# Optimization experiments

Hardware: AMD Instinct MI355X
Metric: run time of the kernel (lower is better)

Reference implementation:

```python
import jax, jax.numpy as jnp
import numpy as np

EMBED_DIM = 1024
NUM_HEADS = 16
HEAD_DIM = EMBED_DIM // NUM_HEADS
SCALE = HEAD_DIM ** -0.5
B, S = 2, 2048


def setup_inputs() -> dict:
    key = jax.random.key(0)
    ks = jax.random.split(key, 11)
    lim = 1.0 / np.sqrt(EMBED_DIM)
    def lin(kw, kb):
        W = jax.random.uniform(kw, (EMBED_DIM, EMBED_DIM), jnp.float32, -lim, lim)
        b = jax.random.uniform(kb, (EMBED_DIM,), jnp.float32, -lim, lim)
        return W, b
    Wq, bq = lin(ks[0], ks[1])
    Wk, bk = lin(ks[2], ks[3])
    Wv, bv = lin(ks[4], ks[5])
    Wo, bo = lin(ks[6], ks[7])
    query = jax.random.normal(ks[8], (B, S, EMBED_DIM), jnp.float32)
    key_t = jax.random.normal(ks[9], (B, S, EMBED_DIM), jnp.float32)
    value = jax.random.normal(ks[10], (B, S, EMBED_DIM), jnp.float32)
    return {"query": query, "key": key_t, "value": value,
            "Wq": Wq, "bq": bq, "Wk": Wk, "bk": bk,
            "Wv": Wv, "bv": bv, "Wo": Wo, "bo": bo}


def reference(query, key, value, Wq, bq, Wk, bk, Wv, bv, Wo, bo):
    # 'flash' path with attn_mask=None == full softmax attention (chunking is
    # only an execution schedule; per-chunk softmax is over the full key axis).
    b, s, _ = query.shape
    def heads(x, W, bias):
        y = x @ W.T + bias                      # [b, s, E]
        return y.reshape(b, s, NUM_HEADS, HEAD_DIM).transpose(0, 2, 1, 3)  # [b, h, s, d]
    q = heads(query, Wq, bq)
    k = heads(key, Wk, bk)
    v = heads(value, Wv, bv)
    scores = jnp.einsum('bhqd,bhkd->bhqk', q, k) * SCALE
    attn = jax.nn.softmax(scores, axis=-1)
    out = jnp.einsum('bhqk,bhkd->bhqd', attn, v)
    out = out.transpose(0, 2, 1, 3).reshape(b, s, EMBED_DIM)
    return out @ Wo.T + bo
```

## Files before the change

### kernel.cpp

```cpp
#include <hip/hip_runtime.h>

typedef unsigned short u16;
typedef unsigned int u32;
typedef __attribute__((ext_vector_type(8))) __bf16 bf16x8;
typedef __attribute__((ext_vector_type(4))) float f32x4;
typedef __attribute__((ext_vector_type(4))) unsigned short u16x4;
typedef __attribute__((ext_vector_type(8))) unsigned short u16x8;
typedef __attribute__((ext_vector_type(4))) unsigned int u32x4;

#define DEV static __device__ __forceinline__

DEV void async_copy16(const void* g, void* l) {
  __builtin_amdgcn_global_load_lds((const __attribute__((address_space(1))) void*)g,
                                   (__attribute__((address_space(3))) void*)l, 16, 0, 0);
}
DEV float b2f(u16 s) { union { unsigned u; float f; } v; v.u = ((unsigned)s) << 16; return v.f; }
DEV u16 f2b(float f) {
  union { float f; unsigned u; } v; v.f = f;
  unsigned r = v.u + 0x7FFFu + ((v.u >> 16) & 1u);
  return (u16)(r >> 16);
}
DEV u32 pack2bf(float a, float b) {
  u32 ua = __float_as_uint(a) + 0x8000u;
  u32 ub = __float_as_uint(b) + 0x8000u;
  return __builtin_amdgcn_perm(ub, ua, 0x07060302u);
}

#define MFMA(a, b, c) __builtin_amdgcn_mfma_f32_16x16x32_bf16((a), (b), (c), 0, 0, 0)

__global__ void detect_dtype(const unsigned* __restrict__ q, int* __restrict__ flag) {
  const int lane = threadIdx.x;
  const unsigned w = q[lane];
  const unsigned e = (w >> 7) & 0xFFu;
  const bool inr = (e >= 100u && e <= 132u);
  const unsigned long long m = __ballot(inr);
  if (lane == 0) flag[0] = (__popcll(m) >= 48) ? 1 : 0;
}

__global__ void convert_inputs(
    const void* s0, const void* s1, const void* s2,
    const void* s3, const void* s4, const void* s5, const void* s6,
    const void* s7, const void* s8, const void* s9, const void* s10,
    u16* __restrict__ d0, u16* __restrict__ d1, u16* __restrict__ d2,
    u16* __restrict__ d3, u16* __restrict__ d4, u16* __restrict__ d5, u16* __restrict__ d6,
    float* __restrict__ e7, float* __restrict__ e8, float* __restrict__ e9, float* __restrict__ e10,
    const int* __restrict__ flag)
{
  const int bi = blockIdx.y;
  const void* src = nullptr; u16* db = nullptr; float* df = nullptr; int n = 0;
  switch (bi) {
    case 0:  src = s0;  db = d0; n = 4194304; break;
    case 1:  src = s1;  db = d1; n = 4194304; break;
    case 2:  src = s2;  db = d2; n = 4194304; break;
    case 3:  src = s3;  db = d3; n = 1048576; break;
    case 4:  src = s4;  db = d4; n = 1048576; break;
    case 5:  src = s5;  db = d5; n = 1048576; break;
    case 6:  src = s6;  db = d6; n = 1048576; break;
    case 7:  src = s7;  df = e7; n = 1024; break;
    case 8:  src = s8;  df = e8; n = 1024; break;
    case 9:  src = s9;  df = e9; n = 1024; break;
    default: src = s10; df = e10; n = 1024; break;
  }
  const int isbf = flag[0];
  const int stride = gridDim.x * 256 * 8;
  for (int i = (blockIdx.x * 256 + threadIdx.x) * 8; i < n; i += stride) {
    if (db) {
      u16x8 v;
      if (isbf) {
        v = *(const u16x8*)((const u16*)src + i);
      } else {
        const float* sf = (const float*)src;
#pragma unroll
        for (int j = 0; j < 8; ++j) v[j] = f2b(sf[i + j]);
      }
      *(u16x8*)(db + i) = v;
    } else {
#pragma unroll
      for (int j = 0; j < 8; ++j) {
        float x = isbf ? b2f(((const u16*)src)[i + j]) : ((const float*)src)[i + j];
        df[i + j] = x;
      }
    }
  }
}

__global__ void gemm_qkv(const u16* __restrict__ X0, const u16* __restrict__ X1, const u16* __restrict__ X2,
                         const u16* __restrict__ W0, const u16* __restrict__ W1, const u16* __restrict__ W2,
                         const float* __restrict__ B0, const float* __restrict__ B1, const float* __restrict__ B2,
                         u16* __restrict__ Y0, u16* __restrict__ Y1, u16* __restrict__ Y2,
                         float* __restrict__ Yf, const int* __restrict__ flag, int mode0)
{
  __shared__ __align__(16) u16 smem[17408];
  u16* As = smem;
  u16* Bs = smem + 4096;

  const int z = blockIdx.z;
  const u16* X  = (z == 0) ? X0 : ((z == 1) ? X1 : X2);
  const u16* W  = (z == 0) ? W0 : ((z == 1) ? W1 : W2);
  const float* Bi = (z == 0) ? B0 : ((z == 1) ? B1 : B2);
  u16* Y        = (z == 0) ? Y0 : ((z == 1) ? Y1 : Y2);
  const int mode = mode0 ? mode0 : z;
  const int outbf = flag[0];

  const int t = threadIdx.x, wave = t >> 6, lane = t & 63;
  const int lane15 = lane & 15, quad = lane >> 4;
  const int m0 = blockIdx.y * 128, n0 = blockIdx.x * 128;

  const u16* gA = X + (size_t)(m0 + wave * 16 + (lane >> 2)) * 1024 + (lane & 3) * 8;
  const u16* gB = W + (size_t)(n0 + wave * 16 + (lane >> 2)) * 1024 + (lane & 3) * 8;
  u16* lA = &As[wave * 16 * 32];
  u16* lB = &Bs[wave * 16 * 32];

  f32x4 acc[4][4];
#pragma unroll
  for (int i = 0; i < 4; ++i)
#pragma unroll
    for (int j = 0; j < 4; ++j) acc[i][j] = (f32x4){0.f, 0.f, 0.f, 0.f};

  const int wr = wave >> 1, wc = wave & 1;

  for (int k0 = 0; k0 < 1024; k0 += 32) {
    async_copy16(gA, lA);
    async_copy16(gA + 64 * 1024, lA + 64 * 32);
    async_copy16(gB, lB);
    async_copy16(gB + 64 * 1024, lB + 64 * 32);
    gA += 32; gB += 32;
    __syncthreads();

    bf16x8 af[4], bfv[4];
#pragma unroll
    for (int mt = 0; mt < 4; ++mt)
      af[mt] = *(const bf16x8*)&As[(wr * 64 + mt * 16 + lane15) * 32 + quad * 8];
#pragma unroll
    for (int nt = 0; nt < 4; ++nt)
      bfv[nt] = *(const bf16x8*)&Bs[(wc * 64 + nt * 16 + lane15) * 32 + quad * 8];
#pragma unroll
    for (int mt = 0; mt < 4; ++mt)
#pragma unroll
      for (int nt = 0; nt < 4; ++nt)
        acc[mt][nt] = MFMA(af[mt], bfv[nt], acc[mt][nt]);
    __syncthreads();
  }

  const float qscale = 0.125f * 1.44269504088896340736f;

  if (mode == 2) {
    u16* T2 = smem;
    __syncthreads();
#pragma unroll
    for (int mt = 0; mt < 4; ++mt) {
      const int sl_base = wr * 64 + mt * 16 + quad * 4;
#pragma unroll
      for (int nt = 0; nt < 4; ++nt) {
        const int nn = wc * 64 + nt * 16 + lane15;
        const float bias_v = Bi[n0 + nn];
#pragma unroll
        for (int r = 0; r < 4; ++r) {
          const int sl = sl_base + r;
          const int sp = ((sl & 15) << 3) | (sl >> 4);
          T2[nn * 136 + sp] = f2b(acc[mt][nt][r] + bias_v);
        }
      }
    }
    __syncthreads();
    const size_t grow0 = (size_t)(m0 >> 11) * 1024 + n0;
    const int col0 = m0 & 2047;
#pragma unroll
    for (int i = 0; i < 8; ++i) {
      const int id = i * 256 + t;
      const int row = id >> 4, ch = id & 15;
      *(u16x8*)&Y[(grow0 + row) * 2048 + col0 + ch * 8] = *(const u16x8*)&T2[row * 136 + ch * 8];
    }
    return;
  }

#pragma unroll
  for (int mt = 0; mt < 4; ++mt) {
    const int m_base = m0 + wr * 64 + mt * 16 + quad * 4;
#pragma unroll
    for (int nt = 0; nt < 4; ++nt) {
      const int n = n0 + wc * 64 + nt * 16 + lane15;
      const float bias_v = Bi[n];
#pragma unroll
      for (int r = 0; r < 4; ++r) {
        const int m = m_base + r;
        float v = acc[mt][nt][r] + bias_v;
        if (mode == 0) v *= qscale;
        if (mode == 3) {
          if (outbf) Y[(size_t)m * 1024 + n] = f2b(v);
          else       Yf[(size_t)m * 1024 + n] = v;
        } else {
          size_t addr = (((size_t)(m >> 11) * 16 + (n >> 6)) * 2048 + (size_t)(m & 2047)) * 64 + (n & 63);
          Y[addr] = f2b(v);
        }
      }
    }
  }
}

__global__ __launch_bounds__(256, 2) void flash_attn(const u16* __restrict__ Qs, const u16* __restrict__ Ks,
                                                     const u16* __restrict__ Vt, u16* __restrict__ AO)
{
  __shared__ __align__(16) u16 smem[32768];
  u16* Kt = smem;
  u16* Vs = smem + 8192;

  const int t = threadIdx.x, wave = t >> 6, lane = t & 63;
  const int lane15 = lane & 15, quad = lane >> 4;
  const int l7 = lane15 & 7;
  const int bh = blockIdx.y;
  const int q0 = blockIdx.x * 128;
  u16* Pw = smem + 16384 + wave * 4096;

  const u16* Qb = Qs + ((size_t)bh * 2048 + q0) * 64;
  const u16* Kb = Ks + (size_t)bh * 2048 * 64;
  const u16* Vb = Vt + (size_t)bh * 64 * 2048;

  const int krow = lane >> 3;
  const int kchunk = (lane & 7) ^ (krow & 7);
  const int vrow = lane >> 4;
  const int vchunk = (lane & 15) ^ (((wave & 1) << 2) + vrow);

#pragma unroll
  for (int r = 0; r < 4; ++r)
    async_copy16(Qb + (size_t)(r * 32 + wave * 8 + krow) * 64 + kchunk * 8,
                 &Kt[(r * 32 + wave * 8) * 64]);
  __syncthreads();
  bf16x8 aq[2][2];
#pragma unroll
  for (int mt = 0; mt < 2; ++mt)
#pragma unroll
    for (int ks = 0; ks < 2; ++ks)
      aq[mt][ks] = *(const bf16x8*)&Kt[(wave * 32 + mt * 16 + lane15) * 64 + ((ks * 4 + quad) ^ l7) * 8];
  __syncthreads();

  f32x4 acc_o[2][4], acc_l[2];
#pragma unroll
  for (int mt = 0; mt < 2; ++mt) {
    acc_l[mt] = (f32x4){0.f, 0.f, 0.f, 0.f};
#pragma unroll
    for (int i = 0; i < 4; ++i) acc_o[mt][i] = (f32x4){0.f, 0.f, 0.f, 0.f};
  }

  u16x8 ou;
#pragma unroll
  for (int j = 0; j < 8; ++j) ou[j] = 0x3F80;
  const bf16x8 ones = __builtin_bit_cast(bf16x8, ou);

  for (int kt = 0; kt < 16; ++kt) {
#pragma unroll
    for (int r = 0; r < 4; ++r)
      async_copy16(Kb + (size_t)(kt * 128 + r * 32 + wave * 8 + krow) * 64 + kchunk * 8,
                   &Kt[(r * 32 + wave * 8) * 64]);
#pragma unroll
    for (int r = 0; r < 4; ++r)
      async_copy16(Vb + (size_t)(r * 16 + wave * 4 + vrow) * 2048 + kt * 128 + vchunk * 8,
                   &Vs[(r * 16 + wave * 4) * 128]);
    __syncthreads();

    f32x4 s[2][8];
#pragma unroll
    for (int mt = 0; mt < 2; ++mt)
#pragma unroll
      for (int nt = 0; nt < 8; ++nt) s[mt][nt] = (f32x4){0.f, 0.f, 0.f, 0.f};
#pragma unroll
    for (int ks = 0; ks < 2; ++ks) {
      bf16x8 bk[8];
#pragma unroll
      for (int nt = 0; nt < 8; ++nt)
        bk[nt] = *(const bf16x8*)&Kt[(nt * 16 + lane15) * 64 + ((ks * 4 + quad) ^ l7) * 8];
#pragma unroll
      for (int mt = 0; mt < 2; ++mt)
#pragma unroll
        for (int nt = 0; nt < 8; ++nt)
          s[mt][nt] = MFMA(aq[mt][ks], bk[nt], s[mt][nt]);
    }

#pragma unroll
    for (int mt = 0; mt < 2; ++mt)
#pragma unroll
      for (int rg = 0; rg < 4; ++rg) {
        u32x4 w;
#pragma unroll
        for (int j = 0; j < 4; ++j)
          w[j] = pack2bf(__builtin_amdgcn_exp2f(s[mt][2 * j][rg]),
                         __builtin_amdgcn_exp2f(s[mt][2 * j + 1][rg]));
        const int r = mt * 16 + quad * 4 + rg;
        *(u32x4*)&Pw[r * 128 + (lane15 ^ (r & 7)) * 8] = w;
      }
    __threadfence_block();

#pragma unroll
    for (int ks2 = 0; ks2 < 4; ++ks2) {
      bf16x8 bv[4], ap[2];
#pragma unroll
      for (int dt = 0; dt < 4; ++dt)
        bv[dt] = *(const bf16x8*)&Vs[(dt * 16 + lane15) * 128 + ((ks2 * 4 + quad) ^ l7) * 8];
#pragma unroll
      for (int mt = 0; mt < 2; ++mt)
        ap[mt] = *(const bf16x8*)&Pw[(mt * 16 + lane15) * 128 + ((ks2 * 4 + quad) ^ l7) * 8];
#pragma unroll
      for (int mt = 0; mt < 2; ++mt) {
#pragma unroll
        for (int dt = 0; dt < 4; ++dt)
          acc_o[mt][dt] = MFMA(ap[mt], bv[dt], acc_o[mt][dt]);
        acc_l[mt] = MFMA(ap[mt], ones, acc_l[mt]);
      }
    }
    __syncthreads();
  }

  float rinv[2][4];
#pragma unroll
  for (int mt = 0; mt < 2; ++mt)
#pragma unroll
    for (int rg = 0; rg < 4; ++rg) rinv[mt][rg] = 1.0f / acc_l[mt][rg];

  u16* T = smem;
#pragma unroll
  for (int mt = 0; mt < 2; ++mt)
#pragma unroll
    for (int dt = 0; dt < 4; ++dt)
#pragma unroll
      for (int rg = 0; rg < 4; ++rg)
        T[(wave * 32 + mt * 16 + quad * 4 + rg) * 72 + dt * 16 + lane15] =
            f2b(acc_o[mt][dt][rg] * rinv[mt][rg]);
  __syncthreads();

  const int b = bh >> 4, h = bh & 15;
#pragma unroll
  for (int i = 0; i < 4; ++i) {
    const int id = i * 256 + t;
    const int row = id >> 3, ch = id & 7;
    *(u16x8*)&AO[((size_t)b * 2048 + q0 + row) * 1024 + h * 64 + ch * 8] =
        *(const u16x8*)&T[row * 72 + ch * 8];
  }
}

extern "C" void kernel_launch(void* const* d_in, const int* in_sizes, int n_in,
                              void* d_out, int out_size, void* d_ws, size_t ws_size,
                              hipStream_t stream)
{
  const void* query = d_in[0];
  const void* key_  = d_in[1];
  const void* value = d_in[2];
  const void* Wq = d_in[3]; const void* bq = d_in[4];
  const void* Wk = d_in[5]; const void* bk = d_in[6];
  const void* Wv = d_in[7]; const void* bv = d_in[8];
  const void* Wo = d_in[9]; const void* bo = d_in[10];

  u16* ws = (u16*)d_ws;
  u16* Qs  = ws;
  u16* Ks  = Qs + 4194304;
  u16* Vt  = Ks + 4194304;
  u16* AO  = Vt + 4194304;
  u16* Xq  = AO + 4194304;
  u16* Xk  = Xq + 4194304;
  u16* Xv  = Xk + 4194304;
  u16* Wqc = Xv + 4194304;
  u16* Wkc = Wqc + 1048576;
  u16* Wvc = Wkc + 1048576;
  u16* Woc = Wvc + 1048576;
  float* Bc = (float*)(Woc + 1048576);
  int* flag = (int*)(Bc + 4096);

  detect_dtype<<<1, 64, 0, stream>>>((const unsigned*)query, flag);
  convert_inputs<<<dim3(128, 11), 256, 0, stream>>>(
      query, key_, value, Wq, Wk, Wv, Wo, bq, bk, bv, bo,
      Xq, Xk, Xv, Wqc, Wkc, Wvc, Woc,
      Bc, Bc + 1024, Bc + 2048, Bc + 3072, flag);

  gemm_qkv<<<dim3(8, 32, 3), 256, 0, stream>>>(Xq, Xk, Xv, Wqc, Wkc, Wvc,
                                               Bc, Bc + 1024, Bc + 2048,
                                               Qs, Ks, Vt, nullptr, flag, 0);
  flash_attn<<<dim3(16, 32), 256, 0, stream>>>(Qs, Ks, Vt, AO);
  gemm_qkv<<<dim3(8, 32, 1), 256, 0, stream>>>(AO, AO, AO, Woc, Woc, Woc,
                                               Bc + 3072, Bc + 3072, Bc + 3072,
                                               (u16*)d_out, (u16*)d_out, (u16*)d_out,
                                               (float*)d_out, flag, 3);
}
```

Before: 232.4 us.

## Double-buffer GEMM LDS tiles and remap block indices for XCD locality

The QKV projection GEMM now uses two LDS buffers. It issues the async global-to-LDS copy for the next K-slice before computing on the current one, which is meant to hide load latency behind MFMA work. Both the GEMM and flash attention kernels also remap the linear block ID so that consecutive work items land on the same XCD (blocks stride by 8), aiming to improve L2 reuse of shared A/W rows and K/V heads. The remapping hardcodes grid sizes of 256 and 512 blocks. It assumes the async copies finish before the barrier, which depends on how the compiler inserts vmcnt waits.

```diff
diff --git a/kernel.cpp b/kernel.cpp
--- a/kernel.cpp
+++ b/kernel.cpp
@@ -91,8 +91,6 @@
                          float* __restrict__ Yf, const int* __restrict__ flag, int mode0)
 {
   __shared__ __align__(16) u16 smem[17408];
-  u16* As = smem;
-  u16* Bs = smem + 4096;
 
   const int z = blockIdx.z;
   const u16* X  = (z == 0) ? X0 : ((z == 1) ? X1 : X2);
@@ -104,12 +102,13 @@
 
   const int t = threadIdx.x, wave = t >> 6, lane = t & 63;
   const int lane15 = lane & 15, quad = lane >> 4;
-  const int m0 = blockIdx.y * 128, n0 = blockIdx.x * 128;
+
+  const int L = blockIdx.y * 8 + blockIdx.x;
+  const int wrk = (L & 7) * 32 + (L >> 3);
+  const int m0 = (wrk >> 3) * 128, n0 = (wrk & 7) * 128;
 
   const u16* gA = X + (size_t)(m0 + wave * 16 + (lane >> 2)) * 1024 + (lane & 3) * 8;
   const u16* gB = W + (size_t)(n0 + wave * 16 + (lane >> 2)) * 1024 + (lane & 3) * 8;
-  u16* lA = &As[wave * 16 * 32];
-  u16* lB = &Bs[wave * 16 * 32];
 
   f32x4 acc[4][4];
 #pragma unroll
@@ -119,26 +118,42 @@
 
   const int wr = wave >> 1, wc = wave & 1;
 
-  for (int k0 = 0; k0 < 1024; k0 += 32) {
+  u16* lA0 = smem + wave * 512;
+  u16* lB0 = smem + 4096 + wave * 512;
+  u16* lA1 = smem + 8192 + wave * 512;
+  u16* lB1 = smem + 12288 + wave * 512;
+
+  auto stage = [&](u16* lA, u16* lB) {
     async_copy16(gA, lA);
     async_copy16(gA + 64 * 1024, lA + 64 * 32);
     async_copy16(gB, lB);
     async_copy16(gB + 64 * 1024, lB + 64 * 32);
     gA += 32; gB += 32;
-    __syncthreads();
-
+  };
+  auto compute = [&](const u16* As_, const u16* Bs_) {
     bf16x8 af[4], bfv[4];
 #pragma unroll
     for (int mt = 0; mt < 4; ++mt)
-      af[mt] = *(const bf16x8*)&As[(wr * 64 + mt * 16 + lane15) * 32 + quad * 8];
+      af[mt] = *(const bf16x8*)&As_[(wr * 64 + mt * 16 + lane15) * 32 + quad * 8];
 #pragma unroll
     for (int nt = 0; nt < 4; ++nt)
-      bfv[nt] = *(const bf16x8*)&Bs[(wc * 64 + nt * 16 + lane15) * 32 + quad * 8];
+      bfv[nt] = *(const bf16x8*)&Bs_[(wc * 64 + nt * 16 + lane15) * 32 + quad * 8];
 #pragma unroll
     for (int mt = 0; mt < 4; ++mt)
 #pragma unroll
       for (int nt = 0; nt < 4; ++nt)
         acc[mt][nt] = MFMA(af[mt], bfv[nt], acc[mt][nt]);
+  };
+
+  stage(lA0, lB0);
+  __syncthreads();
+
+  for (int k0 = 0; k0 < 1024; k0 += 64) {
+    if (k0 + 32 < 1024) stage(lA1, lB1);
+    compute(smem, smem + 4096);
+    __syncthreads();
+    if (k0 + 64 < 1024) stage(lA0, lB0);
+    compute(smem + 8192, smem + 12288);
     __syncthreads();
   }
 
@@ -146,7 +161,6 @@
 
   if (mode == 2) {
     u16* T2 = smem;
-    __syncthreads();
 #pragma unroll
     for (int mt = 0; mt < 4; ++mt) {
       const int sl_base = wr * 64 + mt * 16 + quad * 4;
@@ -208,8 +222,11 @@
   const int t = threadIdx.x, wave = t >> 6, lane = t & 63;
   const int lane15 = lane & 15, quad = lane >> 4;
   const int l7 = lane15 & 7;
-  const int bh = blockIdx.y;
-  const int q0 = blockIdx.x * 128;
+
+  const int Lb = blockIdx.y * 16 + blockIdx.x;
+  const int wrk = (Lb & 7) * 64 + (Lb >> 3);
+  const int bh = wrk >> 4;
+  const int q0 = (wrk & 15) * 128;
   u16* Pw = smem + 16384 + wave * 4096;
 
   const u16* Qb = Qs + ((size_t)bh * 2048 + q0) * 64;
```

Result: faster. 223.4 us (-3.9%).
